# Optimization experiments

Measured on AMD Instinct MI355X. Metric: run time of the kernel, lower is better.

The kernel has to match this reference:

```python
import jax, jax.numpy as jnp
import numpy as np

# Geometry constants matching PointLoss.__init__ defaults
FOV_H = 360.0   # horizontal FOV (deg)
FOV_VU = 3.0    # upper vertical FOV (deg)
DH = 0.5        # delta_h
DV = 0.5        # delta_v
PROJ_H = 52     # int(26 / 0.5)
PROJ_W = 720    # int(360 / 0.5)
THETAC = 0.5    # confidence threshold
LAMDA = 1.0     # fov-loss weight
ANGRATE = 1.0   # anglelossrate
EPS = 1e-8


def setup_inputs() -> dict:
    key = jax.random.key(0)
    ks = jax.random.split(key, 10)
    B, H, W = 64, PROJ_H, PROJ_W
    return {
        "vertexmap_proj": jax.random.normal(ks[0], (B, H, W, 3), jnp.float32),
        "normalmap_proj": jax.random.normal(ks[1], (B, H, W, 3), jnp.float32),
        "uncertainty": jax.random.uniform(ks[2], (B, H, W), jnp.float32),
        "now_normalmap": jax.random.normal(ks[3], (B, H, W, 3), jnp.float32),
        "now_confidencemap": jax.random.uniform(ks[4], (B, H, W), jnp.float32),
        "last_normalmap": jax.random.normal(ks[5], (B, H, W, 3), jnp.float32),
        "last_vertexmap": jax.random.normal(ks[6], (B, H, W, 3), jnp.float32),
        "sx": jnp.zeros((1,), jnp.float32),
        "sq": jnp.zeros((1,), jnp.float32),
        "now_maskmap": jax.random.randint(ks[7], (B, H, W), 0, 2, jnp.int32),
        "last_maskmap": jax.random.randint(ks[8], (B, H, W), 0, 2, jnp.int32),
    }


def _gather_proj(m, flat_idx, B, H, W):
    """Gather pixels of m [B,H,W,(C)] at flat index [B,H,W] -> same shape as m."""
    if m.ndim == 3:
        mf = m.reshape(B, H * W)
        return jnp.take_along_axis(mf, flat_idx.reshape(B, H * W), axis=1).reshape(B, H, W)
    C = m.shape[-1]
    mf = m.reshape(B, H * W, C)
    idx = jnp.broadcast_to(flat_idx.reshape(B, H * W, 1), (B, H * W, C))
    return jnp.take_along_axis(mf, idx, axis=1).reshape(B, H, W, C)


def reference(vertexmap_proj, normalmap_proj, uncertainty, now_normalmap,
              now_confidencemap, last_normalmap, last_vertexmap, sx, sq,
              now_maskmap, last_maskmap):
    B, H, W, _ = vertexmap_proj.shape
    v = vertexmap_proj

    # mask of valid current pixels: maskmap > 0 and normal non-zero
    mask0 = (now_maskmap > 0) & (jnp.sum(jnp.abs(now_normalmap), -1) != 0)

    # spherical re-projection (movegrid=True)
    depth = jnp.sqrt(jnp.sum(v * v, -1) + EPS)
    yaw = jnp.arctan2(v[..., 1], v[..., 0]) * (180.0 / np.pi)
    pitch = jnp.arcsin(jnp.clip(v[..., 2] / depth, -1.0, 1.0)) * (180.0 / np.pi)
    proj_x = (FOV_H / 2 - yaw) / DH
    proj_y = (FOV_VU - pitch) / DV

    # fov loss = masked mse(proj, clamp(proj)) (F.mse_loss default mean)
    m0 = mask0.astype(v.dtype)
    n0 = jnp.maximum(jnp.sum(m0), 1.0)
    fovloss = (jnp.sum(m0 * (proj_x - jnp.clip(proj_x, 0, W - 1)) ** 2)
               + jnp.sum(m0 * (proj_y - jnp.clip(proj_y, 0, H - 1)) ** 2)) / n0

    prx = jnp.round(proj_x)
    pry = jnp.round(proj_y)
    inb = (prx >= 0) & (prx < W) & (pry >= 0) & (pry < H)
    prxi = jnp.clip(prx, 0, W - 1).astype(jnp.int32)
    pryi = jnp.clip(pry, 0, H - 1).astype(jnp.int32)
    flat = pryi * W + prxi  # [B,H,W]

    nl = _gather_proj(last_normalmap, flat, B, H, W)   # last normal at projected pixel
    vl = _gather_proj(last_vertexmap, flat, B, H, W)   # last vertex at projected pixel
    lm = _gather_proj(last_maskmap, flat, B, H, W)

    lastmask = (lm > 0) & (jnp.sum(jnp.abs(nl), -1) != 0)
    mask = mask0 & inb & lastmask & (now_confidencemap >= THETAC)
    m = mask.astype(v.dtype)
    n = jnp.maximum(jnp.sum(m), 1.0)

    # point-to-plane ICP residual, uncertainty-weighted L1
    r = jnp.sum(nl * (v - vl), -1)
    icploss = jnp.sum(m * uncertainty * jnp.abs(r)) / n

    # angular loss: 1 - |cos(angle between normals)|
    nn = normalmap_proj
    cosang = jnp.abs(jnp.sum(nl * nn, -1)) / jnp.sqrt(
        jnp.sum(nl * nl, -1) * jnp.sum(nn * nn, -1) + EPS)
    angloss = jnp.sum(m * uncertainty * (1.0 - cosang)) / n

    sx0, sq0 = sx[0], sq[0]
    total = (jnp.exp(-sx0) * icploss + sx0
             + ANGRATE * jnp.exp(-sq0) * angloss + sq0
             + LAMDA * fovloss)
    return total
```

## Files before the change

### kernel.cpp

```cpp
#include <hip/hip_runtime.h>
#include <math.h>


namespace {
constexpr int B_ = 64, H_ = 52, W_ = 720;
constexpr int HW_ = H_ * W_;
constexpr int NPIX = B_ * HW_;
constexpr int QPI  = HW_ / 4;
constexpr int NQUAD = NPIX / 4;
constexpr int NTHREADS = 256;
constexpr int QPT = 4;
constexpr int NBLOCKS = NQUAD / (NTHREADS * QPT);
constexpr int TSTRIDE = NBLOCKS * NTHREADS;
constexpr float EPSF = 1e-8f;
constexpr float RAD2DEG = 57.29577951308232f;
}
static_assert(NBLOCKS * NTHREADS * QPT == NQUAD, "grid must tile quads exactly");

struct Stream {
    float4 va, vb, vc;
    float4 na, nb, nc;
    int4   mm;
    float4 cf;
};

__global__ __launch_bounds__(NTHREADS) void pointloss_main(
    const float* __restrict__ v,
    const float* __restrict__ nrm,
    const float* __restrict__ unc,
    const float* __restrict__ nown,
    const float* __restrict__ conf,
    const float* __restrict__ lastn,
    const float* __restrict__ lastv,
    const int*   __restrict__ nowm,
    const int*   __restrict__ lastm,
    float* __restrict__ partials)
{
    float s_m0 = 0.f, s_fov = 0.f, s_m = 0.f, s_icp = 0.f, s_ang = 0.f;

    const float4* __restrict__ v4 = (const float4*)v;
    const float4* __restrict__ n4 = (const float4*)nown;
    const float4* __restrict__ r4 = (const float4*)nrm;
    const float4* __restrict__ u4 = (const float4*)unc;
    const int4*   __restrict__ m4 = (const int4*)nowm;
    const float4* __restrict__ c4 = (const float4*)conf;

    const int tid = blockIdx.x * NTHREADS + threadIdx.x;

    auto ld = [&](int q) {
        Stream s;
        s.va = v4[3*q+0]; s.vb = v4[3*q+1]; s.vc = v4[3*q+2];
        s.na = n4[3*q+0]; s.nb = n4[3*q+1]; s.nc = n4[3*q+2];
        s.mm = m4[q];
        s.cf = c4[q];
        return s;
    };

    Stream s = ld(tid);

    #pragma unroll
    for (int it = 0; it < QPT; ++it) {
        const int q = tid + it * TSTRIDE;

        Stream snext;
        if (it < QPT - 1) snext = ld(q + TSTRIDE);

        const int gbase = (q / QPI) * HW_;

        const float vx[4] = {s.va.x, s.va.w, s.vb.z, s.vc.y};
        const float vy[4] = {s.va.y, s.vb.x, s.vb.w, s.vc.z};
        const float vz[4] = {s.va.z, s.vb.y, s.vc.x, s.vc.w};
        const float ax[4] = {s.na.x, s.na.w, s.nb.z, s.nc.y};
        const float ay[4] = {s.na.y, s.nb.x, s.nb.w, s.nc.z};
        const float az[4] = {s.na.z, s.nb.y, s.nc.x, s.nc.w};
        const int   mk[4] = {s.mm.x, s.mm.y, s.mm.z, s.mm.w};
        const float cv[4] = {s.cf.x, s.cf.y, s.cf.z, s.cf.w};

        bool g[4];
        int  gi[4];
        #pragma unroll
        for (int j = 0; j < 4; ++j) {
            const bool mask0 = (mk[j] > 0) &&
                ((fabsf(ax[j]) + fabsf(ay[j]) + fabsf(az[j])) != 0.0f);

            const float depth = sqrtf(vx[j]*vx[j] + vy[j]*vy[j] + vz[j]*vz[j] + EPSF);
            const float yaw   = atan2f(vy[j], vx[j]) * RAD2DEG;
            const float pitch = asinf(fminf(fmaxf(vz[j] / depth, -1.f), 1.f)) * RAD2DEG;
            const float px = (180.0f - yaw) * 2.0f;
            const float py = (3.0f - pitch) * 2.0f;

            if (mask0) {
                const float dx = px - fminf(fmaxf(px, 0.f), (float)(W_ - 1));
                const float dy = py - fminf(fmaxf(py, 0.f), (float)(H_ - 1));
                s_m0  += 1.0f;
                s_fov += dx*dx + dy*dy;
            }

            const float prx = rintf(px), pry = rintf(py);
            const bool inb = (prx >= 0.f) && (prx < (float)W_) &&
                             (pry >= 0.f) && (pry < (float)H_);
            g[j]  = mask0 && inb && (cv[j] >= 0.5f);
            gi[j] = g[j] ? (gbase + (int)pry * W_ + (int)prx) : 0;
        }
        const bool anyg = g[0] | g[1] | g[2] | g[3];

        float4 ra = {0,0,0,0}, rb = {0,0,0,0}, rc = {0,0,0,0}, uq = {0,0,0,0};
        if (anyg) {
            ra = r4[3*q+0]; rb = r4[3*q+1]; rc = r4[3*q+2];
            uq = u4[q];
        }
        float lx[4] = {0,0,0,0}, ly[4] = {0,0,0,0}, lz[4] = {0,0,0,0};
        float wx[4] = {0,0,0,0}, wy[4] = {0,0,0,0}, wz[4] = {0,0,0,0};
        int   lm[4] = {0,0,0,0};
        #pragma unroll
        for (int j = 0; j < 4; ++j) {
            if (g[j]) {
                const int gi3 = 3 * gi[j];
                lx[j] = lastn[gi3+0]; ly[j] = lastn[gi3+1]; lz[j] = lastn[gi3+2];
                lm[j] = lastm[gi[j]];
                wx[j] = lastv[gi3+0]; wy[j] = lastv[gi3+1]; wz[j] = lastv[gi3+2];
            }
        }

        const float nx[4] = {ra.x, ra.w, rb.z, rc.y};
        const float ny[4] = {ra.y, rb.x, rb.w, rc.z};
        const float nz[4] = {ra.z, rb.y, rc.x, rc.w};
        const float uu[4] = {uq.x, uq.y, uq.z, uq.w};

        #pragma unroll
        for (int j = 0; j < 4; ++j) {
            if (g[j] && (lm[j] > 0) &&
                ((fabsf(lx[j]) + fabsf(ly[j]) + fabsf(lz[j])) != 0.f)) {
                const float r  = lx[j]*(vx[j]-wx[j]) + ly[j]*(vy[j]-wy[j])
                               + lz[j]*(vz[j]-wz[j]);
                const float dt = lx[j]*nx[j] + ly[j]*ny[j] + lz[j]*nz[j];
                const float den = (lx[j]*lx[j] + ly[j]*ly[j] + lz[j]*lz[j]) *
                                  (nx[j]*nx[j] + ny[j]*ny[j] + nz[j]*nz[j]) + EPSF;
                const float cosang = fabsf(dt) * rsqrtf(den);
                s_m   += 1.0f;
                s_icp += uu[j] * fabsf(r);
                s_ang += uu[j] * (1.0f - cosang);
            }
        }

        s = snext;
    }

    #pragma unroll
    for (int off = 32; off > 0; off >>= 1) {
        s_m0  += __shfl_down(s_m0,  off);
        s_fov += __shfl_down(s_fov, off);
        s_m   += __shfl_down(s_m,   off);
        s_icp += __shfl_down(s_icp, off);
        s_ang += __shfl_down(s_ang, off);
    }
    __shared__ float red[NTHREADS / 64][5];
    const int lane = threadIdx.x & 63;
    const int wv   = threadIdx.x >> 6;
    if (lane == 0) {
        red[wv][0] = s_m0;  red[wv][1] = s_fov; red[wv][2] = s_m;
        red[wv][3] = s_icp; red[wv][4] = s_ang;
    }
    __syncthreads();
    if (threadIdx.x == 0) {
        float t[5] = {0.f, 0.f, 0.f, 0.f, 0.f};
        for (int w2 = 0; w2 < NTHREADS / 64; ++w2)
            for (int c = 0; c < 5; ++c) t[c] += red[w2][c];
        float* o = partials + blockIdx.x * 5;
        for (int c = 0; c < 5; ++c) o[c] = t[c];
    }
}

__global__ __launch_bounds__(256) void pointloss_finalize(
    const float* __restrict__ partials,
    const float* __restrict__ sx,
    const float* __restrict__ sq,
    float* __restrict__ out)
{
    double a0 = 0, a1 = 0, a2 = 0, a3 = 0, a4 = 0;
    for (int i = threadIdx.x; i < NBLOCKS; i += 256) {
        const float* pp = partials + i * 5;
        a0 += (double)pp[0]; a1 += (double)pp[1]; a2 += (double)pp[2];
        a3 += (double)pp[3]; a4 += (double)pp[4];
    }
    #pragma unroll
    for (int off = 32; off > 0; off >>= 1) {
        a0 += __shfl_down(a0, off);
        a1 += __shfl_down(a1, off);
        a2 += __shfl_down(a2, off);
        a3 += __shfl_down(a3, off);
        a4 += __shfl_down(a4, off);
    }
    __shared__ double red[4][5];
    const int lane = threadIdx.x & 63;
    const int wv   = threadIdx.x >> 6;
    if (lane == 0) {
        red[wv][0] = a0; red[wv][1] = a1; red[wv][2] = a2;
        red[wv][3] = a3; red[wv][4] = a4;
    }
    __syncthreads();
    if (threadIdx.x == 0) {
        double t[5] = {0, 0, 0, 0, 0};
        for (int w2 = 0; w2 < 4; ++w2)
            for (int c = 0; c < 5; ++c) t[c] += red[w2][c];
        const double n0 = fmax(t[0], 1.0);
        const double n  = fmax(t[2], 1.0);
        const double sx0 = (double)sx[0], sq0 = (double)sq[0];
        const double total = exp(-sx0) * (t[3] / n) + sx0
                           + exp(-sq0) * (t[4] / n) + sq0
                           + t[1] / n0;
        out[0] = (float)total;
    }
}

extern "C" void kernel_launch(void* const* d_in, const int* in_sizes, int n_in,
                              void* d_out, int out_size, void* d_ws, size_t ws_size,
                              hipStream_t stream) {
    const float* v     = (const float*)d_in[0];
    const float* nrm   = (const float*)d_in[1];
    const float* unc   = (const float*)d_in[2];
    const float* nown  = (const float*)d_in[3];
    const float* conf  = (const float*)d_in[4];
    const float* lastn = (const float*)d_in[5];
    const float* lastv = (const float*)d_in[6];
    const float* sx    = (const float*)d_in[7];
    const float* sq    = (const float*)d_in[8];
    const int*   nowm  = (const int*)d_in[9];
    const int*   lastm = (const int*)d_in[10];

    float* partials = (float*)d_ws;

    pointloss_main<<<NBLOCKS, NTHREADS, 0, stream>>>(
        v, nrm, unc, nown, conf, lastn, lastv, nowm, lastm, partials);
    pointloss_finalize<<<1, 256, 0, stream>>>(partials, sx, sq, (float*)d_out);
}
```

Baseline: 199.1 us.

## Batch two quads per thread with all loads and gathers issued before compute

Cuts quads per thread from four to two, which doubles the block count. Each thread now loads both streams up front, computes both projections, then issues every gather for both quads before any reduction math. The aim is more memory-level parallelism for the dependent random gathers, so their latencies overlap instead of serialising per iteration. The cost is more live registers per thread, which may lower occupancy, plus twice as many partials to reduce.

Result: no change. 197.4 us (-0.9%).

```diff
diff --git a/kernel.cpp b/kernel.cpp
--- a/kernel.cpp
+++ b/kernel.cpp
@@ -9,7 +9,7 @@
 constexpr int QPI  = HW_ / 4;
 constexpr int NQUAD = NPIX / 4;
 constexpr int NTHREADS = 256;
-constexpr int QPT = 4;
+constexpr int QPT = 2;
 constexpr int NBLOCKS = NQUAD / (NTHREADS * QPT);
 constexpr int TSTRIDE = NBLOCKS * NTHREADS;
 constexpr float EPSF = 1e-8f;
@@ -22,6 +22,21 @@
     float4 na, nb, nc;
     int4   mm;
     float4 cf;
+};
+
+struct Quad {
+    float vx[4], vy[4], vz[4];
+    bool  g[4];
+    int   gi[4];
+    bool  anyg;
+};
+
+struct Gath {
+    float lx[4], ly[4], lz[4];
+    float wx[4], wy[4], wz[4];
+    float nx[4], ny[4], nz[4];
+    float uu[4];
+    int   lm[4];
 };
 
 __global__ __launch_bounds__(NTHREADS) void pointloss_main(
@@ -46,6 +61,8 @@
     const float4* __restrict__ c4 = (const float4*)conf;
 
     const int tid = blockIdx.x * NTHREADS + threadIdx.x;
+    const int q0 = tid;
+    const int q1 = tid + TSTRIDE;
 
     auto ld = [&](int q) {
         Stream s;
@@ -56,17 +73,11 @@
         return s;
     };
 
-    Stream s = ld(tid);
-
-    #pragma unroll
-    for (int it = 0; it < QPT; ++it) {
-        const int q = tid + it * TSTRIDE;
-
-        Stream snext;
-        if (it < QPT - 1) snext = ld(q + TSTRIDE);
-
+    const Stream S0 = ld(q0);
+    const Stream S1 = ld(q1);
+
+    auto phase1 = [&](const Stream& s, int q, Quad& Q) {
         const int gbase = (q / QPI) * HW_;
-
         const float vx[4] = {s.va.x, s.va.w, s.vb.z, s.vc.y};
         const float vy[4] = {s.va.y, s.vb.x, s.vb.w, s.vc.z};
         const float vz[4] = {s.va.z, s.vb.y, s.vc.x, s.vc.w};
@@ -76,8 +87,6 @@
         const int   mk[4] = {s.mm.x, s.mm.y, s.mm.z, s.mm.w};
         const float cv[4] = {s.cf.x, s.cf.y, s.cf.z, s.cf.w};
 
-        bool g[4];
-        int  gi[4];
         #pragma unroll
         for (int j = 0; j < 4; ++j) {
             const bool mask0 = (mk[j] > 0) &&
@@ -99,52 +108,65 @@
             const float prx = rintf(px), pry = rintf(py);
             const bool inb = (prx >= 0.f) && (prx < (float)W_) &&
                              (pry >= 0.f) && (pry < (float)H_);
-            g[j]  = mask0 && inb && (cv[j] >= 0.5f);
-            gi[j] = g[j] ? (gbase + (int)pry * W_ + (int)prx) : 0;
-        }
-        const bool anyg = g[0] | g[1] | g[2] | g[3];
-
+            Q.g[j]  = mask0 && inb && (cv[j] >= 0.5f);
+            Q.gi[j] = Q.g[j] ? (gbase + (int)pry * W_ + (int)prx) : 0;
+            Q.vx[j] = vx[j]; Q.vy[j] = vy[j]; Q.vz[j] = vz[j];
+        }
+        Q.anyg = Q.g[0] | Q.g[1] | Q.g[2] | Q.g[3];
+    };
+
+    Quad Q0, Q1;
+    phase1(S0, q0, Q0);
+    phase1(S1, q1, Q1);
+
+    auto gather = [&](const Quad& Q, int q, Gath& G) {
         float4 ra = {0,0,0,0}, rb = {0,0,0,0}, rc = {0,0,0,0}, uq = {0,0,0,0};
-        if (anyg) {
+        if (Q.anyg) {
             ra = r4[3*q+0]; rb = r4[3*q+1]; rc = r4[3*q+2];
             uq = u4[q];
         }
-        float lx[4] = {0,0,0,0}, ly[4] = {0,0,0,0}, lz[4] = {0,0,0,0};
-        float wx[4] = {0,0,0,0}, wy[4] = {0,0,0,0}, wz[4] = {0,0,0,0};
-        int   lm[4] = {0,0,0,0};
         #pragma unroll
         for (int j = 0; j < 4; ++j) {
-            if (g[j]) {
-                const int gi3 = 3 * gi[j];
-                lx[j] = lastn[gi3+0]; ly[j] = lastn[gi3+1]; lz[j] = lastn[gi3+2];
-                lm[j] = lastm[gi[j]];
-                wx[j] = lastv[gi3+0]; wy[j] = lastv[gi3+1]; wz[j] = lastv[gi3+2];
+            G.lx[j] = 0.f; G.ly[j] = 0.f; G.lz[j] = 0.f;
+            G.wx[j] = 0.f; G.wy[j] = 0.f; G.wz[j] = 0.f;
+            G.lm[j] = 0;
+            if (Q.g[j]) {
+                const int gi3 = 3 * Q.gi[j];
+                G.lx[j] = lastn[gi3+0]; G.ly[j] = lastn[gi3+1]; G.lz[j] = lastn[gi3+2];
+                G.lm[j] = lastm[Q.gi[j]];
+                G.wx[j] = lastv[gi3+0]; G.wy[j] = lastv[gi3+1]; G.wz[j] = lastv[gi3+2];
             }
         }
-
-        const float nx[4] = {ra.x, ra.w, rb.z, rc.y};
-        const float ny[4] = {ra.y, rb.x, rb.w, rc.z};
-        const float nz[4] = {ra.z, rb.y, rc.x, rc.w};
-        const float uu[4] = {uq.x, uq.y, uq.z, uq.w};
-
+        G.nx[0]=ra.x; G.nx[1]=ra.w; G.nx[2]=rb.z; G.nx[3]=rc.y;
+        G.ny[0]=ra.y; G.ny[1]=rb.x; G.ny[2]=rb.w; G.ny[3]=rc.z;
+        G.nz[0]=ra.z; G.nz[1]=rb.y; G.nz[2]=rc.x; G.nz[3]=rc.w;
+        G.uu[0]=uq.x; G.uu[1]=uq.y; G.uu[2]=uq.z; G.uu[3]=uq.w;
+    };
+
+    Gath G0, G1;
+    gather(Q0, q0, G0);
+    gather(Q1, q1, G1);
+
+    auto consume = [&](const Quad& Q, const Gath& G) {
         #pragma unroll
         for (int j = 0; j < 4; ++j) {
-            if (g[j] && (lm[j] > 0) &&
-                ((fabsf(lx[j]) + fabsf(ly[j]) + fabsf(lz[j])) != 0.f)) {
-                const float r  = lx[j]*(vx[j]-wx[j]) + ly[j]*(vy[j]-wy[j])
-                               + lz[j]*(vz[j]-wz[j]);
-                const float dt = lx[j]*nx[j] + ly[j]*ny[j] + lz[j]*nz[j];
-                const float den = (lx[j]*lx[j] + ly[j]*ly[j] + lz[j]*lz[j]) *
-                                  (nx[j]*nx[j] + ny[j]*ny[j] + nz[j]*nz[j]) + EPSF;
+            if (Q.g[j] && (G.lm[j] > 0) &&
+                ((fabsf(G.lx[j]) + fabsf(G.ly[j]) + fabsf(G.lz[j])) != 0.f)) {
+                const float r  = G.lx[j]*(Q.vx[j]-G.wx[j]) + G.ly[j]*(Q.vy[j]-G.wy[j])
+                               + G.lz[j]*(Q.vz[j]-G.wz[j]);
+                const float dt = G.lx[j]*G.nx[j] + G.ly[j]*G.ny[j] + G.lz[j]*G.nz[j];
+                const float den = (G.lx[j]*G.lx[j] + G.ly[j]*G.ly[j] + G.lz[j]*G.lz[j]) *
+                                  (G.nx[j]*G.nx[j] + G.ny[j]*G.ny[j] + G.nz[j]*G.nz[j]) + EPSF;
                 const float cosang = fabsf(dt) * rsqrtf(den);
                 s_m   += 1.0f;
-                s_icp += uu[j] * fabsf(r);
-                s_ang += uu[j] * (1.0f - cosang);
+                s_icp += G.uu[j] * fabsf(r);
+                s_ang += G.uu[j] * (1.0f - cosang);
             }
         }
-
-        s = snext;
-    }
+    };
+
+    consume(Q0, G0);
+    consume(Q1, G1);
 
     #pragma unroll
     for (int off = 32; off > 0; off >>= 1) {
```
